# Kernel optimization log

Measured on AMD Instinct MI355X. Metric: run time of the kernel, lower is better.

The kernel has to match this reference:

```python
import jax, jax.numpy as jnp
import numpy as np

B, N, D = 4, 2048, 768
H, DH = 12, 64  # heads, qk/v head dim
SCALE = DH ** -0.5


def setup_inputs() -> dict:
    key = jax.random.key(0)
    ks = jax.random.split(key, 6)
    s = (1.0 / np.sqrt(D)).astype(np.float32)
    return {
        'x': jax.random.normal(ks[0], (B, N, D), dtype=jnp.float32),
        'x_mask': jax.random.randint(ks[1], (B, N), 0, 2) > 0,
        'Wq': jax.random.normal(ks[2], (D, H * DH), dtype=jnp.float32) * s,
        'Wk': jax.random.normal(ks[3], (D, H * DH), dtype=jnp.float32) * s,
        'Wv': jax.random.normal(ks[4], (D, H * DH), dtype=jnp.float32) * s,
        'Wo': jax.random.normal(ks[5], (H * DH, D), dtype=jnp.float32) * s,
    }


def reference(x, x_mask, Wq, Wk, Wv, Wo):
    # projections (no bias), split heads: b n (h d) -> b h n d
    q = (x @ Wq).reshape(B, N, H, DH).transpose(0, 2, 1, 3)
    k = (x @ Wk).reshape(B, N, H, DH).transpose(0, 2, 1, 3)
    v = (x @ Wv).reshape(B, N, H, DH).transpose(0, 2, 1, 3)
    dots = jnp.einsum('bhid,bhjd->bhij', q, k) * SCALE
    mask_value = -jnp.finfo(dots.dtype).max
    # q_mask [b,1,i,1] & k_mask [b,1,1,j] (self-attention: both from x_mask)
    input_mask = x_mask[:, None, :, None] & x_mask[:, None, None, :]
    dots = jnp.where(input_mask, dots, mask_value)
    attn = jax.nn.softmax(dots.astype(jnp.float32), axis=-1)
    # dropout is identity in eval mode
    out = jnp.einsum('bhij,bhjd->bhid', attn, v)
    out = out.transpose(0, 2, 1, 3).reshape(B, N, H * DH)  # b h n d -> b n (h d)
    return out @ Wo
```

## Files before the change

kernel.cpp:

```cpp
#include <hip/hip_runtime.h>


#define B_ 4
#define N_ 2048
#define D_ 768
#define H_ 12
#define DH_ 64
#define CSC_ 0.18033688011112042f

typedef __attribute__((ext_vector_type(8))) short bf8_t;
typedef __attribute__((ext_vector_type(4))) float f4_t;
typedef __attribute__((ext_vector_type(16))) float f16v;
typedef __attribute__((ext_vector_type(4))) int i4_t;

__device__ __forceinline__ short f2b(float f) {
  union { float f; unsigned u; } v; v.f = f;
  unsigned r = v.u + 0x7FFFu + ((v.u >> 16) & 1u);
  return (short)(r >> 16);
}
__device__ __forceinline__ float b2f(short s) {
  union { unsigned u; float f; } v; v.u = ((unsigned)(unsigned short)s) << 16;
  return v.f;
}
__device__ __forceinline__ unsigned cvtpk(float lo, float hi) {
  unsigned r;
  asm("v_cvt_pk_bf16_f32 %0, %1, %2" : "=v"(r) : "v"(lo), "v"(hi));
  return r;
}
__device__ __forceinline__ void plswap(unsigned& a, unsigned& b) {
  asm("v_permlane32_swap_b32 %0, %1" : "+v"(a), "+v"(b));
}
__device__ __forceinline__ float max3f(float a, float b, float c) {
  float r;
  asm("v_max3_f32 %0, %1, %2, %3" : "=v"(r) : "v"(a), "v"(b), "v"(c));
  return r;
}

#define GLOAD_LDS16(gp, lp)                                                       \
  __builtin_amdgcn_global_load_lds(                                               \
      (const __attribute__((address_space(1))) void*)(gp),                        \
      (__attribute__((address_space(3))) void*)(lp), 16, 0, 0)

__global__ __launch_bounds__(256) void k_convx(const float* __restrict__ x,
                                               short* __restrict__ xb) {
  int i = blockIdx.x * 256 + threadIdx.x;
  int base = i * 8;
  float4 a = *(const float4*)(x + base);
  float4 b = *(const float4*)(x + base + 4);
  bf8_t v;
  v[0] = f2b(a.x); v[1] = f2b(a.y); v[2] = f2b(a.z); v[3] = f2b(a.w);
  v[4] = f2b(b.x); v[5] = f2b(b.y); v[6] = f2b(b.z); v[7] = f2b(b.w);
  *(bf8_t*)(xb + base) = v;
}

__global__ __launch_bounds__(256) void k_wtrans(const float* __restrict__ Wq,
                                                const float* __restrict__ Wk,
                                                const float* __restrict__ Wv,
                                                const float* __restrict__ Wo,
                                                short* __restrict__ WqkvT,
                                                short* __restrict__ WoT) {
  int z = blockIdx.z;
  const float* W = (z == 0) ? Wq : (z == 1) ? Wk : (z == 2) ? Wv : Wo;
  short* dst = (z < 3) ? (WqkvT + (size_t)z * D_ * D_) : WoT;
  float sc = (z == 0) ? CSC_ : 1.f;
  __shared__ float T[64][65];
  int r0 = blockIdx.y * 64, c0 = blockIdx.x * 64;
  int tr = threadIdx.x >> 6, tc = threadIdx.x & 63;
#pragma unroll
  for (int i = 0; i < 16; ++i) {
    int r = tr + i * 4;
    T[r][tc] = W[(size_t)(r0 + r) * D_ + c0 + tc];
  }
  __syncthreads();
#pragma unroll
  for (int i = 0; i < 16; ++i) {
    int r = tr + i * 4;
    dst[(size_t)(c0 + r) * D_ + r0 + tc] = f2b(T[tc][r] * sc);
  }
}

template <int MODE>
__global__ __launch_bounds__(256) void k_gemm(const short* __restrict__ A,
                                              const short* __restrict__ BT, int K,
                                              short* __restrict__ Qb, short* __restrict__ Kb,
                                              short* __restrict__ Vb,
                                              float* __restrict__ Cout, int ldc) {
  __shared__ short As[128 * 72];
  __shared__ short Bs[128 * 72];
  int row0 = blockIdx.y * 128, col0 = blockIdx.x * 128;
  int tid = threadIdx.x, lane = tid & 63, w = tid >> 6;
  int wr = w >> 1, wc = w & 1;
  int lr = lane & 15, lhi = lane >> 4;
  f4_t acc[4][4];
#pragma unroll
  for (int mi = 0; mi < 4; ++mi)
#pragma unroll
    for (int ni = 0; ni < 4; ++ni) acc[mi][ni] = (f4_t){0.f, 0.f, 0.f, 0.f};

  bf8_t ra[4], rb[4];

#pragma unroll
  for (int cc = 0; cc < 4; ++cc) {
    int c = tid + cc * 256, r = c >> 3, c8 = (c & 7) * 8;
    ra[cc] = *(const bf8_t*)(A + (size_t)(row0 + r) * K + c8);
    rb[cc] = *(const bf8_t*)(BT + (size_t)(col0 + r) * K + c8);
  }
#pragma unroll
  for (int cc = 0; cc < 4; ++cc) {
    int c = tid + cc * 256, r = c >> 3, c8 = (c & 7) * 8;
    *(bf8_t*)(As + r * 72 + c8) = ra[cc];
    *(bf8_t*)(Bs + r * 72 + c8) = rb[cc];
  }
  __syncthreads();

  int nt = K / 64;
  for (int t = 0; t < nt; ++t) {
    if (t + 1 < nt) {
      int k0 = (t + 1) * 64;
#pragma unroll
      for (int cc = 0; cc < 4; ++cc) {
        int c = tid + cc * 256, r = c >> 3, c8 = (c & 7) * 8;
        ra[cc] = *(const bf8_t*)(A + (size_t)(row0 + r) * K + k0 + c8);
        rb[cc] = *(const bf8_t*)(BT + (size_t)(col0 + r) * K + k0 + c8);
      }
    }
#pragma unroll
    for (int kc = 0; kc < 2; ++kc) {
      bf8_t av[4], bv[4];
#pragma unroll
      for (int mi = 0; mi < 4; ++mi)
        av[mi] = *(const bf8_t*)(As + (64 * wr + 16 * mi + lr) * 72 + kc * 32 + lhi * 8);
#pragma unroll
      for (int ni = 0; ni < 4; ++ni)
        bv[ni] = *(const bf8_t*)(Bs + (64 * wc + 16 * ni + lr) * 72 + kc * 32 + lhi * 8);
#pragma unroll
      for (int mi = 0; mi < 4; ++mi)
#pragma unroll
        for (int ni = 0; ni < 4; ++ni)
          acc[mi][ni] = __builtin_amdgcn_mfma_f32_16x16x32_bf16(av[mi], bv[ni], acc[mi][ni], 0, 0, 0);
    }
    __syncthreads();
    if (t + 1 < nt) {
#pragma unroll
      for (int cc = 0; cc < 4; ++cc) {
        int c = tid + cc * 256, r = c >> 3, c8 = (c & 7) * 8;
        *(bf8_t*)(As + r * 72 + c8) = ra[cc];
        *(bf8_t*)(Bs + r * 72 + c8) = rb[cc];
      }
      __syncthreads();
    }
  }
#pragma unroll
  for (int mi = 0; mi < 4; ++mi)
#pragma unroll
    for (int ni = 0; ni < 4; ++ni)
#pragma unroll
      for (int r = 0; r < 4; ++r) {
        int row = row0 + 64 * wr + 16 * mi + 4 * lhi + r;
        int col = col0 + 64 * wc + 16 * ni + lr;
        float v = acc[mi][ni][r];
        if (MODE == 0) {
          int which = col / 768;
          int cc2 = col - which * 768;
          int h = cc2 >> 6, dh = cc2 & 63;
          int b = row >> 11, n = row & 2047;
          size_t dst = (((size_t)(b * H_ + h)) * N_ + n) * DH_ + dh;
          short bv2 = f2b(v);
          if (which == 0) Qb[dst] = bv2;
          else if (which == 1) Kb[dst] = bv2;
          else Vb[dst] = bv2;
        } else {
          Cout[(size_t)row * ldc + col] = v;
        }
      }
}

__global__ __launch_bounds__(256) void k_maskidx(const int* __restrict__ xmask,
                                                 int* __restrict__ idx,
                                                 int* __restrict__ cnt) {
  int b = blockIdx.x, t = threadIdx.x;
  const int* mp = xmask + b * N_;
  int loc[8], c = 0;
#pragma unroll
  for (int j = 0; j < 8; ++j) {
    int n = t * 8 + j;
    if (mp[n]) loc[c++] = n;
  }
  __shared__ int sc[256];
  sc[t] = c;
  __syncthreads();
  for (int off = 1; off < 256; off <<= 1) {
    int v = (t >= off) ? sc[t - off] : 0;
    __syncthreads();
    sc[t] += v;
    __syncthreads();
  }
  int base = sc[t] - c;
  int* op = idx + b * N_;
  for (int j = 0; j < c; ++j) op[base + j] = loc[j];
  if (t == 255) cnt[b] = sc[255];
}

__global__ __launch_bounds__(256) void k_vmeanA(const short* __restrict__ Vb,
                                                float* __restrict__ part) {
  int bh = blockIdx.y, ch = blockIdx.x, t = threadIdx.x;
  int rg = t >> 3, cg = t & 7;
  const short* vp = Vb + ((size_t)bh * N_ + ch * 256 + rg) * DH_ + cg * 8;
  float a[8] = {0, 0, 0, 0, 0, 0, 0, 0};
#pragma unroll
  for (int k = 0; k < 8; ++k) {
    bf8_t v = *(const bf8_t*)(vp + (size_t)32 * k * DH_);
#pragma unroll
    for (int e = 0; e < 8; ++e) a[e] += b2f(v[e]);
  }
  __shared__ float red[8][32][8];
#pragma unroll
  for (int e = 0; e < 8; ++e) red[cg][rg][e] = a[e];
  __syncthreads();
  if (t < 64) {
    int g = t >> 3, j = t & 7;
    float s = 0;
#pragma unroll
    for (int i = 0; i < 32; ++i) s += red[g][i][j];
    part[((size_t)bh * 8 + ch) * 64 + g * 8 + j] = s;
  }
}

__global__ __launch_bounds__(256) void k_vmeanB(const float* __restrict__ part,
                                                float* __restrict__ Vmean) {
  int i = blockIdx.x * 256 + threadIdx.x;
  if (i >= 48 * 64) return;
  int bh = i >> 6, dh = i & 63;
  float s = 0;
#pragma unroll
  for (int c = 0; c < 8; ++c) s += part[((size_t)bh * 8 + c) * 64 + dh];
  Vmean[i] = s * (1.f / 2048.f);
}

__global__ __launch_bounds__(256) void k_gather(const short* __restrict__ Kb,
                                                const short* __restrict__ Vb,
                                                const int* __restrict__ idx,
                                                const int* __restrict__ cnt,
                                                short* __restrict__ Kc,
                                                short* __restrict__ Vtc) {
  int bh = blockIdx.y, b = bh / H_;
  int j0 = blockIdx.x * 64;
  int cn = cnt[b];
  int cp = (cn + 63) & ~63;
  if (j0 >= cp) return;
  int t = threadIdx.x;
  __shared__ int sidx[64];
  __shared__ short vt[64][72];
  if (t < 64) sidx[t] = (j0 + t < cn) ? idx[b * N_ + j0 + t] : -1;
  __syncthreads();
  int r = t >> 2, c16 = (t & 3) * 16;
  int src = sidx[r];
  const bf8_t zz = {0, 0, 0, 0, 0, 0, 0, 0};
#pragma unroll
  for (int u = 0; u < 2; ++u) {
    bf8_t kv = (src >= 0) ? *(const bf8_t*)(Kb + ((size_t)bh * N_ + src) * DH_ + c16 + u * 8) : zz;
    bf8_t vv = (src >= 0) ? *(const bf8_t*)(Vb + ((size_t)bh * N_ + src) * DH_ + c16 + u * 8) : zz;
    *(bf8_t*)(Kc + ((size_t)bh * N_ + j0 + r) * DH_ + c16 + u * 8) = kv;
    *(bf8_t*)(&vt[r][c16 + u * 8]) = vv;
  }
  __syncthreads();
  int dh = t >> 2;
#pragma unroll
  for (int u = 0; u < 2; ++u) {
    bf8_t ov;
#pragma unroll
    for (int e = 0; e < 8; ++e) ov[e] = vt[c16 + u * 8 + e][dh];
    *(bf8_t*)(Vtc + ((size_t)bh * DH_ + dh) * N_ + j0 + c16 + u * 8) = ov;
  }
}

__global__ __launch_bounds__(256) void k_fill(const int* __restrict__ xmask,
                                              const float* __restrict__ Vmean,
                                              short* __restrict__ Ao) {
  int b = blockIdx.y;
  int n = blockIdx.x * 32 + (threadIdx.x >> 3);
  int cg = threadIdx.x & 7;
  if (xmask[b * N_ + n]) return;
#pragma unroll
  for (int k = 0; k < 12; ++k) {
    int col = cg * 8 + k * 64;
    int h = col >> 6, dh = col & 63;
    const float* vp = Vmean + ((size_t)b * H_ + h) * 64 + dh;
    bf8_t ov;
#pragma unroll
    for (int e = 0; e < 8; ++e) ov[e] = f2b(vp[e]);
    *(bf8_t*)(Ao + ((size_t)b * N_ + n) * D_ + col) = ov;
  }
}

__global__ __launch_bounds__(256, 3) void k_attn(const short* __restrict__ Q,
                                                 const short* __restrict__ Kcg,
                                                 const short* __restrict__ Vtcg,
                                                 const int* __restrict__ idx,
                                                 const int* __restrict__ cnt,
                                                 short* __restrict__ Aout) {
  int bh = blockIdx.y;
  int b = bh / H_, h = bh - b * H_;
  int cn = cnt[b];
  int nqt = (cn + 127) >> 7;
  if ((int)blockIdx.x >= nqt) return;
  int nkt = (cn + 63) >> 6;
  const short* Qp = Q + (size_t)bh * N_ * DH_;
  const short* Kp = Kcg + (size_t)bh * N_ * DH_;
  const short* Vp = Vtcg + (size_t)bh * DH_ * N_;
  const int* ip = idx + b * N_;
  int q0 = blockIdx.x * 128;
  int tid = threadIdx.x, lane = tid & 63, w = tid >> 6;
  int lq = lane & 31, hi = lane >> 5;

  __shared__ char smem[32768];

  int qrow = q0 + 32 * w + lq;
  int qn = ip[qrow < cn ? qrow : cn - 1];

  bf8_t qf[4];
#pragma unroll
  for (int kc = 0; kc < 4; ++kc)
    qf[kc] = *(const bf8_t*)(Qp + (size_t)qn * DH_ + 16 * kc + 8 * hi);

  short NEGBIG = f2b(-1e30f);
  bf8_t qbf = {hi ? (short)0 : (short)0x3F80, 0, 0, 0, 0, 0, 0, 0};

  f16v acco[2];
#pragma unroll
  for (int i = 0; i < 16; ++i) { acco[0][i] = 0.f; acco[1][i] = 0.f; }
  float m = -1e29f, lsum = 0.f;

  auto STAGE = [&](int key0, int buf) {
    char* kb_ = smem + buf * 16384;
    char* vb_ = kb_ + 8192;
    int row = tid >> 3;
    int cb = (tid & 7) * 16;
    char* lk = kb_ + ((tid >> 6) << 10);
    char* lv = vb_ + ((tid >> 6) << 10);
#pragma unroll
    for (int rr = 0; rr < 2; ++rr) {
      int r2 = row + rr * 32;
      int sw = cb ^ ((r2 & 7) << 4);
      GLOAD_LDS16((const char*)(Kp + (size_t)(key0 + r2) * DH_) + sw, lk + rr * 4096);
      GLOAD_LDS16((const char*)(Vp + (size_t)r2 * N_ + key0) + sw, lv + rr * 4096);
    }
  };

  STAGE(0, 0);
  __syncthreads();

  for (int kt = 0; kt < nkt; ++kt) {
    int cur = kt & 1;
    if (kt + 1 < nkt) STAGE((kt + 1) * 64, cur ^ 1);

    const char* kbase = smem + cur * 16384;
    const char* vbase = kbase + 8192;
    int key0 = kt * 64;

    f16v accs[2];
#pragma unroll
    for (int i = 0; i < 16; ++i) { accs[0][i] = 0.f; accs[1][i] = 0.f; }
    int swz = (lq & 7) << 4;
    __builtin_amdgcn_s_setprio(1);
#pragma unroll
    for (int kc = 0; kc < 4; ++kc) {
      int colb = (32 * kc + 16 * hi) ^ swz;
      bf8_t k0 = *(const bf8_t*)(kbase + lq * 128 + colb);
      bf8_t k1 = *(const bf8_t*)(kbase + (32 + lq) * 128 + colb);
      accs[0] = __builtin_amdgcn_mfma_f32_32x32x16_bf16(k0, qf[kc], accs[0], 0, 0, 0);
      accs[1] = __builtin_amdgcn_mfma_f32_32x32x16_bf16(k1, qf[kc], accs[1], 0, 0, 0);
    }
    __builtin_amdgcn_s_setprio(0);
    if (key0 + 64 > cn) {
      bf8_t bf0 = {(hi || key0 + lq < cn) ? (short)0 : NEGBIG, 0, 0, 0, 0, 0, 0, 0};
      bf8_t bf1 = {(hi || key0 + 32 + lq < cn) ? (short)0 : NEGBIG, 0, 0, 0, 0, 0, 0, 0};
      accs[0] = __builtin_amdgcn_mfma_f32_32x32x16_bf16(bf0, qbf, accs[0], 0, 0, 0);
      accs[1] = __builtin_amdgcn_mfma_f32_32x32x16_bf16(bf1, qbf, accs[1], 0, 0, 0);
    }

    float mx = max3f(accs[0][0], accs[0][1], accs[0][2]);
#pragma unroll
    for (int i = 3; i < 15; i += 2) mx = max3f(mx, accs[0][i], accs[0][i + 1]);
    mx = max3f(mx, accs[0][15], accs[1][0]);
#pragma unroll
    for (int i = 1; i < 15; i += 2) mx = max3f(mx, accs[1][i], accs[1][i + 1]);
    mx = fmaxf(mx, accs[1][15]);
    mx = fmaxf(mx, __shfl_xor(mx, 32));
    if (!__all(mx <= m + 8.f)) {
      float mnew = fmaxf(m, mx);
      float sc = __builtin_amdgcn_exp2f(m - mnew);
      m = mnew;
      lsum *= sc;
#pragma unroll
      for (int i = 0; i < 16; ++i) { acco[0][i] *= sc; acco[1][i] *= sc; }
    }
    float psa[4] = {0.f, 0.f, 0.f, 0.f};
#pragma unroll
    for (int kb2 = 0; kb2 < 2; ++kb2)
#pragma unroll
      for (int r = 0; r < 16; ++r) {
        float p = __builtin_amdgcn_exp2f(accs[kb2][r] - m);
        accs[kb2][r] = p;
        psa[r & 3] += p;
      }
    float ps = (psa[0] + psa[1]) + (psa[2] + psa[3]);
    ps += __shfl_xor(ps, 32);
    lsum += ps;

    __builtin_amdgcn_s_setprio(1);
#pragma unroll
    for (int kc = 0; kc < 4; ++kc) {
      int kb2 = kc >> 1, rb = (kc & 1) * 8;
      unsigned a_ = cvtpk(accs[kb2][rb + 0], accs[kb2][rb + 1]);
      unsigned b_ = cvtpk(accs[kb2][rb + 4], accs[kb2][rb + 5]);
      unsigned c_ = cvtpk(accs[kb2][rb + 2], accs[kb2][rb + 3]);
      unsigned d_ = cvtpk(accs[kb2][rb + 6], accs[kb2][rb + 7]);
      plswap(a_, b_);
      plswap(c_, d_);
      union { i4_t i; bf8_t v; } pu;
      pu.i = (i4_t){(int)a_, (int)c_, (int)b_, (int)d_};
      int colb = (32 * kc + 16 * hi) ^ swz;
      bf8_t v0 = *(const bf8_t*)(vbase + lq * 128 + colb);
      bf8_t v1 = *(const bf8_t*)(vbase + (32 + lq) * 128 + colb);
      acco[0] = __builtin_amdgcn_mfma_f32_32x32x16_bf16(v0, pu.v, acco[0], 0, 0, 0);
      acco[1] = __builtin_amdgcn_mfma_f32_32x32x16_bf16(v1, pu.v, acco[1], 0, 0, 0);
    }
    __builtin_amdgcn_s_setprio(0);

    __syncthreads();
  }
  __syncthreads();

  float inv = 1.f / lsum;
  unsigned* Os = (unsigned*)smem + w * 1152;
#pragma unroll
  for (int dhb = 0; dhb < 2; ++dhb)
#pragma unroll
    for (int r = 0; r < 16; r += 2) {
      unsigned pk = cvtpk(acco[dhb][r] * inv, acco[dhb][r + 1] * inv);
      int colu = 16 * dhb + ((r & 3) >> 1) + 4 * (r >> 2) + 2 * hi;
      Os[lq * 36 + colu] = pk;
    }
#pragma unroll
  for (int it = 0; it < 4; ++it) {
    int q = (lane >> 3) + 8 * it;
    int qr2 = q0 + 32 * w + q;
    if (qr2 < cn) {
      int n = ip[qr2];
      i4_t vv = *(const i4_t*)(Os + q * 36 + 4 * (lane & 7));
      union { i4_t i; bf8_t s; } u2;
      u2.i = vv;
      size_t off = ((size_t)b * N_ + n) * D_ + h * DH_ + 8 * (lane & 7);
      *(bf8_t*)(Aout + off) = u2.s;
    }
  }
}

extern "C" void kernel_launch(void* const* d_in, const int* in_sizes, int n_in,
                              void* d_out, int out_size, void* d_ws, size_t ws_size,
                              hipStream_t stream) {
  (void)in_sizes; (void)n_in; (void)out_size; (void)ws_size;
  const float* x  = (const float*)d_in[0];
  const int*   xm = (const int*)d_in[1];
  const float* Wq = (const float*)d_in[2];
  const float* Wk = (const float*)d_in[3];
  const float* Wv = (const float*)d_in[4];
  const float* Wo = (const float*)d_in[5];
  float* out = (float*)d_out;
  char* ws = (char*)d_ws;

  short* x_bf  = (short*)(ws + 0);
  short* Ao    = (short*)(ws + 0);
  short* WqkvT = (short*)(ws + 12582912);
  int*   idxb  = (int*)(ws + 12582912);
  int*   cntb  = (int*)(ws + 12615680);
  float* part  = (float*)(ws + 12615744);
  float* Vmean = (float*)(ws + 12714048);
  short* WoT   = (short*)(ws + 16121856);
  short* Qb    = (short*)(ws + 17301504);
  short* Kb    = (short*)(ws + 29884416);
  short* Vb    = (short*)(ws + 42467328);
  short* Kc    = (short*)(ws + 55050240);
  short* Vtc   = (short*)(ws + 67633152);

  k_convx<<<3072, 256, 0, stream>>>(x, x_bf);
  k_wtrans<<<dim3(12, 12, 4), 256, 0, stream>>>(Wq, Wk, Wv, Wo, WqkvT, WoT);
  k_gemm<0><<<dim3(18, 64), 256, 0, stream>>>(x_bf, WqkvT, 768, Qb, Kb, Vb, nullptr, 0);
  k_maskidx<<<4, 256, 0, stream>>>(xm, idxb, cntb);
  k_vmeanA<<<dim3(8, 48), 256, 0, stream>>>(Vb, part);
  k_vmeanB<<<12, 256, 0, stream>>>(part, Vmean);
  k_gather<<<dim3(32, 48), 256, 0, stream>>>(Kb, Vb, idxb, cntb, Kc, Vtc);
  k_attn<<<dim3(16, 48), 256, 0, stream>>>(Qb, Kc, Vtc, idxb, cntb, Ao);
  k_fill<<<dim3(64, 4), 256, 0, stream>>>(xm, Vmean, Ao);
  k_gemm<1><<<dim3(6, 64), 256, 0, stream>>>(Ao, WoT, 768, nullptr, nullptr, nullptr, out, 768);
}
```

Measured before the change: 136.0 us.

## Fuse fp32-to-bf16 conversion of x into QKV GEMM loads and swizzle workgroups

Drops the separate x conversion kernel. The QKV GEMM now reads fp32 x directly and packs it to bf16 with v_cvt_pk_bf16_f32 before the LDS store, which removes one launch and one round trip of the bf16 copy of x through memory. It also adds a workgroup index swizzle that spreads consecutive blocks across 8 groups, presumably to match XCD placement and improve L2 reuse. In exchange, each GEMM block loads twice as many bytes for A per tile, and x tiles are re-read in fp32 by all 18 column blocks.

```diff
diff --git a/kernel.cpp b/kernel.cpp
--- a/kernel.cpp
+++ b/kernel.cpp
@@ -40,18 +40,6 @@
   __builtin_amdgcn_global_load_lds(                                               \
       (const __attribute__((address_space(1))) void*)(gp),                        \
       (__attribute__((address_space(3))) void*)(lp), 16, 0, 0)
-
-__global__ __launch_bounds__(256) void k_convx(const float* __restrict__ x,
-                                               short* __restrict__ xb) {
-  int i = blockIdx.x * 256 + threadIdx.x;
-  int base = i * 8;
-  float4 a = *(const float4*)(x + base);
-  float4 b = *(const float4*)(x + base + 4);
-  bf8_t v;
-  v[0] = f2b(a.x); v[1] = f2b(a.y); v[2] = f2b(a.z); v[3] = f2b(a.w);
-  v[4] = f2b(b.x); v[5] = f2b(b.y); v[6] = f2b(b.z); v[7] = f2b(b.w);
-  *(bf8_t*)(xb + base) = v;
-}
 
 __global__ __launch_bounds__(256) void k_wtrans(const float* __restrict__ Wq,
                                                 const float* __restrict__ Wk,
@@ -79,15 +67,21 @@
   }
 }
 
-template <int MODE>
-__global__ __launch_bounds__(256) void k_gemm(const short* __restrict__ A,
+template <int MODE, int AFP32>
+__global__ __launch_bounds__(256) void k_gemm(const void* __restrict__ Ain,
                                               const short* __restrict__ BT, int K,
                                               short* __restrict__ Qb, short* __restrict__ Kb,
                                               short* __restrict__ Vb,
                                               float* __restrict__ Cout, int ldc) {
   __shared__ short As[128 * 72];
   __shared__ short Bs[128 * 72];
-  int row0 = blockIdx.y * 128, col0 = blockIdx.x * 128;
+  int gx = gridDim.x;
+  int nwg = gx * gridDim.y;
+  int flat = blockIdx.y * gx + blockIdx.x;
+  int cpx = nwg >> 3;
+  int swzb = (flat & 7) * cpx + (flat >> 3);
+  int row0 = (swzb / gx) * 128, col0 = (swzb % gx) * 128;
+
   int tid = threadIdx.x, lane = tid & 63, w = tid >> 6;
   int wr = w >> 1, wc = w & 1;
   int lr = lane & 15, lhi = lane >> 4;
@@ -97,18 +91,33 @@
 #pragma unroll
     for (int ni = 0; ni < 4; ++ni) acc[mi][ni] = (f4_t){0.f, 0.f, 0.f, 0.f};
 
+  const float* Af = (const float*)Ain;
+  const short* Ab = (const short*)Ain;
+  float4 raf0[4], raf1[4];
   bf8_t ra[4], rb[4];
 
 #pragma unroll
   for (int cc = 0; cc < 4; ++cc) {
     int c = tid + cc * 256, r = c >> 3, c8 = (c & 7) * 8;
-    ra[cc] = *(const bf8_t*)(A + (size_t)(row0 + r) * K + c8);
+    if (AFP32) {
+      raf0[cc] = *(const float4*)(Af + (size_t)(row0 + r) * K + c8);
+      raf1[cc] = *(const float4*)(Af + (size_t)(row0 + r) * K + c8 + 4);
+    } else {
+      ra[cc] = *(const bf8_t*)(Ab + (size_t)(row0 + r) * K + c8);
+    }
     rb[cc] = *(const bf8_t*)(BT + (size_t)(col0 + r) * K + c8);
   }
 #pragma unroll
   for (int cc = 0; cc < 4; ++cc) {
     int c = tid + cc * 256, r = c >> 3, c8 = (c & 7) * 8;
-    *(bf8_t*)(As + r * 72 + c8) = ra[cc];
+    if (AFP32) {
+      union { i4_t i; bf8_t v; } u;
+      u.i = (i4_t){(int)cvtpk(raf0[cc].x, raf0[cc].y), (int)cvtpk(raf0[cc].z, raf0[cc].w),
+                   (int)cvtpk(raf1[cc].x, raf1[cc].y), (int)cvtpk(raf1[cc].z, raf1[cc].w)};
+      *(bf8_t*)(As + r * 72 + c8) = u.v;
+    } else {
+      *(bf8_t*)(As + r * 72 + c8) = ra[cc];
+    }
     *(bf8_t*)(Bs + r * 72 + c8) = rb[cc];
   }
   __syncthreads();
@@ -120,7 +129,12 @@
 #pragma unroll
       for (int cc = 0; cc < 4; ++cc) {
         int c = tid + cc * 256, r = c >> 3, c8 = (c & 7) * 8;
-        ra[cc] = *(const bf8_t*)(A + (size_t)(row0 + r) * K + k0 + c8);
+        if (AFP32) {
+          raf0[cc] = *(const float4*)(Af + (size_t)(row0 + r) * K + k0 + c8);
+          raf1[cc] = *(const float4*)(Af + (size_t)(row0 + r) * K + k0 + c8 + 4);
+        } else {
+          ra[cc] = *(const bf8_t*)(Ab + (size_t)(row0 + r) * K + k0 + c8);
+        }
         rb[cc] = *(const bf8_t*)(BT + (size_t)(col0 + r) * K + k0 + c8);
       }
     }
@@ -144,7 +158,14 @@
 #pragma unroll
       for (int cc = 0; cc < 4; ++cc) {
         int c = tid + cc * 256, r = c >> 3, c8 = (c & 7) * 8;
-        *(bf8_t*)(As + r * 72 + c8) = ra[cc];
+        if (AFP32) {
+          union { i4_t i; bf8_t v; } u;
+          u.i = (i4_t){(int)cvtpk(raf0[cc].x, raf0[cc].y), (int)cvtpk(raf0[cc].z, raf0[cc].w),
+                       (int)cvtpk(raf1[cc].x, raf1[cc].y), (int)cvtpk(raf1[cc].z, raf1[cc].w)};
+          *(bf8_t*)(As + r * 72 + c8) = u.v;
+        } else {
+          *(bf8_t*)(As + r * 72 + c8) = ra[cc];
+        }
         *(bf8_t*)(Bs + r * 72 + c8) = rb[cc];
       }
       __syncthreads();
@@ -470,7 +491,6 @@
   float* out = (float*)d_out;
   char* ws = (char*)d_ws;
 
-  short* x_bf  = (short*)(ws + 0);
   short* Ao    = (short*)(ws + 0);
   short* WqkvT = (short*)(ws + 12582912);
   int*   idxb  = (int*)(ws + 12582912);
@@ -484,14 +504,13 @@
   short* Kc    = (short*)(ws + 55050240);
   short* Vtc   = (short*)(ws + 67633152);
 
-  k_convx<<<3072, 256, 0, stream>>>(x, x_bf);
   k_wtrans<<<dim3(12, 12, 4), 256, 0, stream>>>(Wq, Wk, Wv, Wo, WqkvT, WoT);
-  k_gemm<0><<<dim3(18, 64), 256, 0, stream>>>(x_bf, WqkvT, 768, Qb, Kb, Vb, nullptr, 0);
+  k_gemm<0, 1><<<dim3(18, 64), 256, 0, stream>>>(x, WqkvT, 768, Qb, Kb, Vb, nullptr, 0);
   k_maskidx<<<4, 256, 0, stream>>>(xm, idxb, cntb);
   k_vmeanA<<<dim3(8, 48), 256, 0, stream>>>(Vb, part);
   k_vmeanB<<<12, 256, 0, stream>>>(part, Vmean);
   k_gather<<<dim3(32, 48), 256, 0, stream>>>(Kb, Vb, idxb, cntb, Kc, Vtc);
   k_attn<<<dim3(16, 48), 256, 0, stream>>>(Qb, Kc, Vtc, idxb, cntb, Ao);
   k_fill<<<dim3(64, 4), 256, 0, stream>>>(xm, Vmean, Ao);
-  k_gemm<1><<<dim3(6, 64), 256, 0, stream>>>(Ao, WoT, 768, nullptr, nullptr, nullptr, out, 768);
-}
+  k_gemm<1, 0><<<dim3(6, 64), 256, 0, stream>>>(Ao, WoT, 768, nullptr, nullptr, nullptr, out, 768);
+}
```

New measurement: 134.0 us. Within noise of the previous version (-1.5%).
